# Kernel optimization log

Measured on AMD Instinct MI355X. Metric: run time of the kernel, lower is better.

## Reference

```python
import jax, jax.numpy as jnp
import numpy as np

EPS = 1e-8
LN_EPS = 1e-5  # torch LayerNorm default


def _ln(x, axes):
    m = jnp.mean(x, axis=axes, keepdims=True)
    v = jnp.var(x, axis=axes, keepdims=True)
    return (x - m) * jax.lax.rsqrt(v + LN_EPS)


def _l2(x):
    # sqrt(sum(x^2, -1, keepdim=True))
    return jnp.sqrt(jnp.sum(x * x, axis=-1, keepdims=True))


def _get_zs(x, Wk, bk, Wv, bv):
    # x: [B,L,Din]
    z = jax.nn.elu(x @ Wk.T + bk)                         # [B,L,D]
    s = jnp.einsum('blp,blq->blpq', z, x @ Wv.T + bv)     # [B,L,D,D]
    z = _ln(jnp.cumsum(z, axis=1) + EPS, -1)
    s = _ln(jnp.cumsum(s, axis=1) + EPS, (-2, -1))
    return z, s


def setup_inputs() -> dict:
    key = jax.random.key(0)
    ks = jax.random.split(key, 10)
    B, L, Din, D, U, PL, SL = 32, 200, 256, 64, 10000, 8, 8
    f32 = jnp.float32
    return {
        'user_id': jax.random.randint(ks[0], (B,), 0, U + 1),
        'seqs_emb': jax.random.normal(ks[1], (B, L, Din), dtype=f32),
        'P': jax.random.normal(ks[2], (B, PL, Din), dtype=f32),
        'S': jax.random.normal(ks[3], (B, SL, Din), dtype=f32),
        'prev_z': jax.random.normal(ks[4], (U + 1, D), dtype=f32),
        'prev_s': jax.random.normal(ks[5], (U + 1, D, D), dtype=f32),
        'Wq': jax.random.normal(ks[6], (D, Din), dtype=f32) / Din,
        'bq': jnp.zeros((D,), f32),
        'Wk': jax.random.normal(ks[7], (D, Din), dtype=f32) / Din,
        'bk': jnp.zeros((D,), f32),
        'Wv': jax.random.normal(ks[8], (D, Din), dtype=f32) / Din,
        'bv': jnp.zeros((D,), f32),
    }


def reference(user_id, seqs_emb, P, S, prev_z, prev_s, Wq, bq, Wk, bk, Wv, bv):
    sg = jax.lax.stop_gradient
    q = jax.nn.elu(seqs_emb @ Wq.T + bq)                  # [B,L,D]
    nq = q / sg(_l2(q) + EPS)
    z, s = _get_zs(seqs_emb, Wk, bk, Wv, bv)
    # plasticity prompt P: add last-step state
    Pz, Ps = _get_zs(P, Wk, bk, Wv, bv)
    z = z + Pz[:, -1:, :]
    s = s + Ps[:, -1:, :, :]
    NAM = _ln(s / sg(_l2(z)[..., None] + EPS) + EPS, (-2, -1))  # [B,L,D,D]
    NA = jnp.einsum('blp,blpq->blq', nq, NAM)
    # per-user recurrent history (use_history=True), with stability prompt S
    pz = prev_z[user_id]                                  # [B,D]
    ps = prev_s[user_id]                                  # [B,D,D]
    mask = (jnp.sum(pz, axis=-1) != 0).astype(NA.dtype)   # [B]
    Sz, Ss = _get_zs(S, Wk, bk, Wv, bv)
    zu = pz + Sz[:, -1, :]
    su = ps + Ss[:, -1, :, :]
    prev_NAM = su / sg(_l2(zu)[..., None] + EPS)          # [B,D,D]
    prev_NA = jnp.einsum('blp,bpq->blq', nq, prev_NAM) * mask[:, None, None]
    NA = _ln(NA + prev_NA, -1)                            # NA_layernorm (dropout p=0)
    std = jnp.std(q / jnp.maximum(z, 1e-6), ddof=1)       # torch.std is unbiased
    return NA, std
```

## Files before the change

kernel.cpp:

```cpp
#include <hip/hip_runtime.h>
#include <math.h>

#define B_   32
#define L_   200
#define DIN_ 256
#define D_   64
#define PL_  8

#define OFF_WT    0
#define OFF_Q     49152
#define OFF_NQ    458752
#define OFF_Z     868352
#define OFF_V     1277952
#define OFF_SZ    1687552
#define OFF_SV    1693952
#define OFF_SNQ   1700352
#define OFF_PZL   1706752
#define OFF_PSL   1708800
#define OFF_PNAM  1839872
#define OFF_MPS2  1970944
#define OFF_H     1970976
#define OFF_C     1977376
#define OFF_CM    1983776
#define OFF_CR    1990176
#define OFF_CCP   1996576
#define OFF_SYR   2002976
#define OFF_SY2R  2009376
#define OFF_ZC    2015776
#define OFF_CP    2425376
#define OFF_T1    2450976
#define OFF_T2    2860576
#define OFF_NAP   3270176

__device__ __forceinline__ float wsum(float x){
#pragma unroll
  for (int o = 32; o > 0; o >>= 1) x += __shfl_xor(x, o, 64);
  return x;
}
__device__ __forceinline__ float eluf(float x){ return x > 0.f ? x : expm1f(x); }

__global__ __launch_bounds__(256) void k_transpose(const float* __restrict__ Wq,
    const float* __restrict__ Wk, const float* __restrict__ Wv, float* __restrict__ wt){
  int idx = blockIdx.x*256 + threadIdx.x;
  if (idx >= 3*16384) return;
  int m = idx >> 14, r = idx & 16383, i = r >> 6, d = r & 63;
  const float* W = (m==0) ? Wq : ((m==1) ? Wk : Wv);
  wt[m*16384 + i*64 + d] = W[d*256 + i];
}

__global__ __launch_bounds__(256) void k_qzv(const float* __restrict__ x, const float* __restrict__ Wt,
    const float* __restrict__ bq, const float* __restrict__ bk, const float* __restrict__ bv,
    float* __restrict__ q, float* __restrict__ nq, float* __restrict__ z, float* __restrict__ v,
    float* __restrict__ sz, float* __restrict__ sv, float* __restrict__ snq){
  __shared__ float xs[16*256];
  int row0 = blockIdx.x * 16;
  int tid = threadIdx.x, d = tid & 63, g = tid >> 6;
  for (int k = tid; k < 4096; k += 256) xs[k] = x[row0*256 + k];
  __syncthreads();
  const float* Wtq = Wt;
  const float* Wtk = Wt + 16384;
  const float* Wtv = Wt + 32768;
  float aq[4] = {0,0,0,0}, ak[4] = {0,0,0,0}, av[4] = {0,0,0,0};
  for (int i = 0; i < 256; i++){
    float wq = Wtq[i*64+d], wk = Wtk[i*64+d], wv = Wtv[i*64+d];
#pragma unroll
    for (int j = 0; j < 4; j++){
      float xv = xs[(g+4*j)*256 + i];
      aq[j] = fmaf(xv, wq, aq[j]);
      ak[j] = fmaf(xv, wk, ak[j]);
      av[j] = fmaf(xv, wv, av[j]);
    }
  }
  float bqd = bq[d], bkd = bk[d], bvd = bv[d];
#pragma unroll
  for (int j = 0; j < 4; j++){
    int r = row0 + g + 4*j;
    float qv = eluf(aq[j] + bqd);
    float zv = eluf(ak[j] + bkd);
    float vv = av[j] + bvd;
    float sq2 = wsum(qv*qv);
    float sq1 = wsum(qv);
    float szv = wsum(zv);
    float svv = wsum(vv);
    float inv = 1.f / (sqrtf(sq2) + 1e-8f);
    q[r*64+d] = qv; nq[r*64+d] = qv*inv; z[r*64+d] = zv; v[r*64+d] = vv;
    if (d == 0){ sz[r] = szv; sv[r] = svv; snq[r] = sq1*inv; }
  }
}

__global__ __launch_bounds__(256) void k_prompt(const float* __restrict__ P, const float* __restrict__ Sp,
    const int* __restrict__ uid, const float* __restrict__ prev_z, const float* __restrict__ prev_s,
    const float* __restrict__ Wt, const float* __restrict__ bk, const float* __restrict__ bv,
    float* __restrict__ PzL, float* __restrict__ PsL, float* __restrict__ mps2, float* __restrict__ pNAM){
  int g = blockIdx.x, b = g & 31, path = g >> 5;
  int tid = threadIdx.x;
  __shared__ float xs[2048];
  __shared__ float zs[512], vs[512];
  __shared__ float red[4];
  __shared__ float facs;
  const float* src = path ? Sp : P;
  for (int k = tid; k < 2048; k += 256) xs[k] = src[b*2048 + k];
  __syncthreads();
  const float* Wtk = Wt + 16384;
  const float* Wtv = Wt + 32768;
  for (int idx = tid; idx < 512; idx += 256){
    int t = idx >> 6, d = idx & 63;
    float ak = 0.f, av = 0.f;
    for (int i = 0; i < 256; i++){
      float xv = xs[t*256+i];
      ak = fmaf(xv, Wtk[i*64+d], ak);
      av = fmaf(xv, Wtv[i*64+d], av);
    }
    zs[idx] = eluf(ak + bk[d]); vs[idx] = av + bv[d];
  }
  __syncthreads();
  float spv[16];
  float l1 = 0.f, l2 = 0.f;
  int p = tid >> 2, q0 = (tid & 3) * 16;
#pragma unroll
  for (int k = 0; k < 16; k++){
    int qq = q0 + k;
    float sp = 0.f;
#pragma unroll
    for (int t = 0; t < 8; t++) sp = fmaf(zs[t*64+p], vs[t*64+qq], sp);
    spv[k] = sp; l1 += sp; l2 += sp*sp;
  }
  float tot0, tot1;
  {
    float val = wsum(l1);
    if ((tid & 63) == 0) red[tid >> 6] = val;
    __syncthreads();
    tot0 = red[0] + red[1] + red[2] + red[3];
    __syncthreads();
    val = wsum(l2);
    if ((tid & 63) == 0) red[tid >> 6] = val;
    __syncthreads();
    tot1 = red[0] + red[1] + red[2] + red[3];
  }
  float mP = tot0 * (1.f/4096.f);
  float varP = tot1 * (1.f/4096.f) - mP*mP;
  float invv = rsqrtf(varP + 1e-5f);
  if (path == 0){
    if (tid == 0) mps2[b] = varP * invv * invv;
    if (tid < 64){
      int d = tid;
      float zc = 0.f;
#pragma unroll
      for (int t = 0; t < 8; t++) zc += zs[t*64+d];
      float s1 = wsum(zc), s2 = wsum(zc*zc);
      float mz = s1*(1.f/64.f), vz = s2*(1.f/64.f) - mz*mz;
      PzL[b*64+d] = (zc - mz) * rsqrtf(vz + 1e-5f);
    }
#pragma unroll
    for (int k = 0; k < 16; k++){
      int o = p*64 + q0 + k;
      PsL[b*4096 + o] = (spv[k] - mP) * invv;
    }
  } else {
    int u = uid[b];
    if (tid < 64){
      int d = tid;
      float zc = 0.f;
#pragma unroll
      for (int t = 0; t < 8; t++) zc += zs[t*64+d];
      float s1 = wsum(zc), s2 = wsum(zc*zc);
      float mz = s1*(1.f/64.f), vz = s2*(1.f/64.f) - mz*mz;
      float szl = (zc - mz) * rsqrtf(vz + 1e-5f);
      float pzv = prev_z[u*64 + d];
      float zu = pzv + szl;
      float zl2 = wsum(zu*zu);
      float psumv = wsum(pzv);
      float fac = ((psumv != 0.f) ? 1.f : 0.f) / (sqrtf(zl2) + 1e-8f);
      if (d == 0) facs = fac;
    }
    __syncthreads();
    float fac = facs;
    const float* psrow = prev_s + (size_t)u * 4096;
#pragma unroll
    for (int k = 0; k < 16; k++){
      int o = p*64 + q0 + k;
      pNAM[b*4096 + o] = (psrow[o] + (spv[k] - mP) * invv) * fac;
    }
  }
}

__global__ __launch_bounds__(256) void k_gram64(const float* __restrict__ z, const float* __restrict__ v,
    const float* __restrict__ nq,
    float* __restrict__ colpart, float* __restrict__ harr, float* __restrict__ NAP){
  __shared__ float smem[20480];
  float* zlT = smem;
  float* vlT = smem + 4096;
  float* nlT = smem + 8192;
  float* ztT = smem + 12288;
  float* vtT = smem + 16384;
  int bid = blockIdx.x;
  int b = bid / 10, pi = bid % 10;
  int rt, ct;
  if (pi < 1){ rt = 0; ct = 0; }
  else if (pi < 3){ rt = 1; ct = pi - 1; }
  else if (pi < 6){ rt = 2; ct = pi - 3; }
  else { rt = 3; ct = pi - 6; }
  int l0 = rt*64, t0 = ct*64;
  int tid = threadIdx.x;
  const float* zb = z + b*12800;
  const float* vb = v + b*12800;
  const float* nb = nq + b*12800;
  {
    int r = tid & 63, kq = tid >> 6;
    int l = l0 + r, t = t0 + r;
    bool lv = l < L_, tv = t < L_;
#pragma unroll
    for (int m = 0; m < 4; m++){
      int k0 = kq*16 + m*4;
      float4 zr4 = lv ? *(const float4*)(zb + l*64 + k0) : make_float4(0,0,0,0);
      float4 vr4 = lv ? *(const float4*)(vb + l*64 + k0) : make_float4(0,0,0,0);
      float4 nr4 = lv ? *(const float4*)(nb + l*64 + k0) : make_float4(0,0,0,0);
      float4 zc4 = tv ? *(const float4*)(zb + t*64 + k0) : make_float4(0,0,0,0);
      float4 vc4 = tv ? *(const float4*)(vb + t*64 + k0) : make_float4(0,0,0,0);
      zlT[(k0+0)*64+r]=zr4.x; zlT[(k0+1)*64+r]=zr4.y; zlT[(k0+2)*64+r]=zr4.z; zlT[(k0+3)*64+r]=zr4.w;
      vlT[(k0+0)*64+r]=vr4.x; vlT[(k0+1)*64+r]=vr4.y; vlT[(k0+2)*64+r]=vr4.z; vlT[(k0+3)*64+r]=vr4.w;
      nlT[(k0+0)*64+r]=nr4.x; nlT[(k0+1)*64+r]=nr4.y; nlT[(k0+2)*64+r]=nr4.z; nlT[(k0+3)*64+r]=nr4.w;
      ztT[(k0+0)*64+r]=zc4.x; ztT[(k0+1)*64+r]=zc4.y; ztT[(k0+2)*64+r]=zc4.z; ztT[(k0+3)*64+r]=zc4.w;
      vtT[(k0+0)*64+r]=vc4.x; vtT[(k0+1)*64+r]=vc4.y; vtT[(k0+2)*64+r]=vc4.z; vtT[(k0+3)*64+r]=vc4.w;
    }
  }
  __syncthreads();
  int rg = tid >> 4, cg = tid & 15;
  int r0 = rg*4, c0 = cg*4;
  float az[16], av[16], an[16];
#pragma unroll
  for (int i = 0; i < 16; i++){ az[i]=0.f; av[i]=0.f; an[i]=0.f; }
  for (int k = 0; k < 64; k++){
    float4 zr4 = *(const float4*)&zlT[k*64 + r0];
    float4 vr4 = *(const float4*)&vlT[k*64 + r0];
    float4 nr4 = *(const float4*)&nlT[k*64 + r0];
    float4 zc4 = *(const float4*)&ztT[k*64 + c0];
    float4 vc4 = *(const float4*)&vtT[k*64 + c0];
    float zr[4] = {zr4.x, zr4.y, zr4.z, zr4.w};
    float vr[4] = {vr4.x, vr4.y, vr4.z, vr4.w};
    float nr[4] = {nr4.x, nr4.y, nr4.z, nr4.w};
    float zc[4] = {zc4.x, zc4.y, zc4.z, zc4.w};
    float vc[4] = {vc4.x, vc4.y, vc4.z, vc4.w};
#pragma unroll
    for (int i = 0; i < 4; i++){
#pragma unroll
      for (int j = 0; j < 4; j++){
        az[i*4+j] = fmaf(zr[i], zc[j], az[i*4+j]);
        av[i*4+j] = fmaf(vr[i], vc[j], av[i*4+j]);
        an[i*4+j] = fmaf(nr[i], zc[j], an[i*4+j]);
      }
    }
  }
  bool diag = (rt == ct);
  float prow[4];
#pragma unroll
  for (int i = 0; i < 4; i++){
    float s = 0.f;
#pragma unroll
    for (int j = 0; j < 4; j++){
      bool keep = !diag || (c0 + j <= r0 + i);
      if (keep) s += az[i*4+j] * av[i*4+j];
    }
    prow[i] = s;
  }
#pragma unroll
  for (int o = 1; o < 16; o <<= 1){
#pragma unroll
    for (int i = 0; i < 4; i++) prow[i] += __shfl_xor(prow[i], o, 64);
  }
  if (cg == 0){
#pragma unroll
    for (int i = 0; i < 4; i++){
      int l = l0 + r0 + i;
      if (l < L_) colpart[(b*L_ + l)*4 + ct] = prow[i];
    }
  }
  if (diag && rg == cg){
#pragma unroll
    for (int i = 0; i < 4; i++){
      int l = l0 + r0 + i;
      if (l < L_) harr[b*L_ + l] = az[i*4+i] * av[i*4+i];
    }
  }
  __syncthreads();
  float* scsT = nlT;
#pragma unroll
  for (int j = 0; j < 4; j++){
    int c = c0 + j;
    float m0 = (!diag || c <= r0+0) ? an[0*4+j] : 0.f;
    float m1 = (!diag || c <= r0+1) ? an[1*4+j] : 0.f;
    float m2 = (!diag || c <= r0+2) ? an[2*4+j] : 0.f;
    float m3 = (!diag || c <= r0+3) ? an[3*4+j] : 0.f;
    *(float4*)&scsT[c*64 + r0] = make_float4(m0, m1, m2, m3);
  }
  __syncthreads();
  int d0 = c0;
  float o4[16];
#pragma unroll
  for (int i = 0; i < 16; i++) o4[i] = 0.f;
#pragma unroll 2
  for (int c = 0; c < 64; c++){
    float4 s4 = *(const float4*)&scsT[c*64 + r0];
    int t = t0 + c; if (t > L_-1) t = L_-1;
    float4 v4 = *(const float4*)(vb + t*64 + d0);
    float sv[4] = {s4.x, s4.y, s4.z, s4.w};
    float vv[4] = {v4.x, v4.y, v4.z, v4.w};
#pragma unroll
    for (int i = 0; i < 4; i++){
#pragma unroll
      for (int j = 0; j < 4; j++) o4[i*4+j] = fmaf(sv[i], vv[j], o4[i*4+j]);
    }
  }
  float* nap = NAP + ((size_t)((b*4 + rt)*4 + ct))*4096;
#pragma unroll
  for (int i = 0; i < 4; i++)
    *(float4*)&nap[(r0+i)*64 + d0] = make_float4(o4[i*4+0], o4[i*4+1], o4[i*4+2], o4[i*4+3]);
}

#define PADK 68
__global__ __launch_bounds__(256) void k_t12(const float* __restrict__ z, const float* __restrict__ v,
    const float* __restrict__ nq, const float* __restrict__ PsL, const float* __restrict__ pNAM,
    float* __restrict__ carr, float* __restrict__ T1, float* __restrict__ T2){
  int b = blockIdx.x / 7, rtile = blockIdx.x % 7;
  int l0 = rtile * 32;
  int tid = threadIdx.x;
  __shared__ float zl[32*PADK], vl[32*PADK];
  __shared__ float nqt[32*65];
  for (int k = tid; k < 2048; k += 256){
    int r = k >> 6, d = k & 63, lr = l0 + r;
    bool ok = lr < L_;
    zl[r*PADK+d]  = ok ? z[(b*L_+lr)*64 + d] : 0.f;
    vl[r*PADK+d]  = ok ? v[(b*L_+lr)*64 + d] : 0.f;
    nqt[r*65+d]   = ok ? nq[(b*L_+lr)*64 + d] : 0.f;
  }
  __syncthreads();
  {
    int w = tid >> 6, lane = tid & 63;
    float wacc[8] = {0,0,0,0,0,0,0,0};
    const float* psb = PsL + b*4096 + lane*64;
    for (int qq = 0; qq < 64; qq += 4){
      float4 p4 = *(const float4*)(psb + qq);
#pragma unroll
      for (int r8 = 0; r8 < 8; r8++){
        float4 v4 = *(const float4*)&vl[(w*8+r8)*PADK+qq];
        wacc[r8] += p4.x*v4.x + p4.y*v4.y + p4.z*v4.z + p4.w*v4.w;
      }
    }
#pragma unroll
    for (int r8 = 0; r8 < 8; r8++){
      int rr = w*8 + r8, l = l0 + rr;
      float c = wsum(zl[rr*PADK+lane] * wacc[r8]);
      if (lane == 0 && l < L_) carr[b*L_ + l] = c;
    }
  }
  int r = tid & 31, c8 = tid >> 5, c0 = c8 * 8;
  float t1a[8] = {0,0,0,0,0,0,0,0}, t2a[8] = {0,0,0,0,0,0,0,0};
  const float* psm = PsL + b*4096;
  const float* pnm = pNAM + b*4096;
  for (int pp = 0; pp < 64; pp++){
    float nv = nqt[r*65 + pp];
    float4 a0 = *(const float4*)(psm + pp*64 + c0);
    float4 a1 = *(const float4*)(psm + pp*64 + c0 + 4);
    float4 b0 = *(const float4*)(pnm + pp*64 + c0);
    float4 b1 = *(const float4*)(pnm + pp*64 + c0 + 4);
    t1a[0] = fmaf(nv, a0.x, t1a[0]); t1a[1] = fmaf(nv, a0.y, t1a[1]);
    t1a[2] = fmaf(nv, a0.z, t1a[2]); t1a[3] = fmaf(nv, a0.w, t1a[3]);
    t1a[4] = fmaf(nv, a1.x, t1a[4]); t1a[5] = fmaf(nv, a1.y, t1a[5]);
    t1a[6] = fmaf(nv, a1.z, t1a[6]); t1a[7] = fmaf(nv, a1.w, t1a[7]);
    t2a[0] = fmaf(nv, b0.x, t2a[0]); t2a[1] = fmaf(nv, b0.y, t2a[1]);
    t2a[2] = fmaf(nv, b0.z, t2a[2]); t2a[3] = fmaf(nv, b0.w, t2a[3]);
    t2a[4] = fmaf(nv, b1.x, t2a[4]); t2a[5] = fmaf(nv, b1.y, t2a[5]);
    t2a[6] = fmaf(nv, b1.z, t2a[6]); t2a[7] = fmaf(nv, b1.w, t2a[7]);
  }
  int l = l0 + r;
  if (l < L_){
    float* t1p = T1 + (b*L_+l)*64 + c0;
    float* t2p = T2 + (b*L_+l)*64 + c0;
    *(float4*)(t1p)     = make_float4(t1a[0], t1a[1], t1a[2], t1a[3]);
    *(float4*)(t1p + 4) = make_float4(t1a[4], t1a[5], t1a[6], t1a[7]);
    *(float4*)(t2p)     = make_float4(t2a[0], t2a[1], t2a[2], t2a[3]);
    *(float4*)(t2p + 4) = make_float4(t2a[4], t2a[5], t2a[6], t2a[7]);
  }
}

__global__ __launch_bounds__(64) void k_cumsum(const float* __restrict__ z,
    const float* __restrict__ sz, const float* __restrict__ sv,
    const float* __restrict__ colpart, const float* __restrict__ harr, const float* __restrict__ carr,
    float* __restrict__ Zcum, float* __restrict__ cM, float* __restrict__ cR, float* __restrict__ cC){
  int b = blockIdx.x, lane = threadIdx.x;
  const float* zb = z + b*12800;
  float* Zb = Zcum + b*12800;
  float Zc = 0.f;
  for (int l = 0; l < 200; l += 4){
    float a0 = zb[(l+0)*64+lane];
    float a1 = zb[(l+1)*64+lane];
    float a2 = zb[(l+2)*64+lane];
    float a3 = zb[(l+3)*64+lane];
    Zc += a0; Zb[(l+0)*64+lane] = Zc;
    Zc += a1; Zb[(l+1)*64+lane] = Zc;
    Zc += a2; Zb[(l+2)*64+lane] = Zc;
    Zc += a3; Zb[(l+3)*64+lane] = Zc;
  }
  float carryM = 0.f, carryR = 0.f, carryC = 0.f;
#pragma unroll
  for (int c = 0; c < 4; c++){
    int l = c*64 + lane;
    bool valid = l < 200;
    int row = b*200 + l;
    float tcol = 0.f;
    if (valid){
      int ltile = l >> 6;
#pragma unroll
      for (int j = 0; j < 4; j++)
        if (j <= ltile) tcol += colpart[row*4 + j];
    }
    float tm = valid ? sz[row]*sv[row] : 0.f;
    float tr = valid ? 2.f*tcol - harr[row] : 0.f;
    float tc = valid ? carr[row] : 0.f;
#pragma unroll
    for (int o = 1; o < 64; o <<= 1){
      float y0 = __shfl_up(tm, o, 64);
      float y1 = __shfl_up(tr, o, 64);
      float y2 = __shfl_up(tc, o, 64);
      if (lane >= o){ tm += y0; tr += y1; tc += y2; }
    }
    tm += carryM; tr += carryR; tc += carryC;
    if (valid){ cM[row] = tm; cR[row] = tr; cC[row] = tc; }
    carryM = __shfl(tm, 63, 64);
    carryR = __shfl(tr, 63, 64);
    carryC = __shfl(tc, 63, 64);
  }
}

__global__ __launch_bounds__(64) void k_finred(const float* __restrict__ q, const float* __restrict__ Zcum,
    const float* __restrict__ PzL, const float* __restrict__ mps2, const float* __restrict__ snq,
    const float* __restrict__ cM, const float* __restrict__ cR, const float* __restrict__ cC,
    const float* __restrict__ T1, const float* __restrict__ T2, const float* __restrict__ NAP,
    float* __restrict__ out, float* __restrict__ Syr, float* __restrict__ Sy2r){
  int row = blockIdx.x;
  int b = row / 200, l = row % 200;
  int lane = threadIdx.x;
  int rt = l >> 6, r = l & 63;
  const float* np_ = NAP + ((size_t)((b*4 + rt)*4))*4096 + r*64 + lane;
  float acc = 0.f;
  for (int ct = 0; ct <= rt; ct++) acc += np_[ct*4096];
  float zc = Zcum[row*64 + lane];
  float s1 = wsum(zc), s2 = wsum(zc*zc);
  float mz = s1*(1.f/64.f), vz = s2*(1.f/64.f) - mz*mz;
  float zf = (zc - mz) * rsqrtf(vz + 1e-5f) + PzL[b*64 + lane];
  float zl2 = wsum(zf*zf);
  float a = sqrtf(zl2) + 1e-8f;
  float m = cM[row] * (1.f/4096.f);
  float var = cR[row] * (1.f/4096.f) - m*m;
  float inv = rsqrtf(var + 1e-5f);
  float varT = inv*inv*var + 2.f*inv*cC[row]*(1.f/4096.f) + mps2[b];
  float invT = rsqrtf(varT + 1e-5f*a*a);
  float cAv = invT*inv;
  float cBv = invT*inv*m*snq[row];
  float cCv = invT;
  float y = q[row*64 + lane] / fmaxf(zf, 1e-6f);
  float ys = wsum(y), ys2 = wsum(y*y);
  if (lane == 0){ Syr[row] = ys; Sy2r[row] = ys2; }
  float NA1 = cAv*acc - cBv + cCv*T1[row*64 + lane] + T2[row*64 + lane];
  float r1 = wsum(NA1), r2 = wsum(NA1*NA1);
  float mm = r1*(1.f/64.f), vv = r2*(1.f/64.f) - mm*mm;
  out[row*64 + lane] = (NA1 - mm) * rsqrtf(vv + 1e-5f);
}

__global__ __launch_bounds__(256) void k_std(const float* __restrict__ Syr, const float* __restrict__ Sy2r,
    float* __restrict__ out){
  __shared__ float redA[4], redB[4];
  int tid = threadIdx.x, lane = tid & 63, g = tid >> 6;
  float a = 0.f, b2 = 0.f;
  for (int i = tid; i < 6400; i += 256){ a += Syr[i]; b2 += Sy2r[i]; }
  a = wsum(a); b2 = wsum(b2);
  if (lane == 0){ redA[g] = a; redB[g] = b2; }
  __syncthreads();
  if (tid == 0){
    float A = redA[0]+redA[1]+redA[2]+redA[3];
    float B2 = redB[0]+redB[1]+redB[2]+redB[3];
    const float N = 409600.f;
    float var = (B2 - A*A/N) / (N - 1.f);
    out[409600] = sqrtf(fmaxf(var, 0.f));
  }
}

extern "C" void kernel_launch(void* const* d_in, const int* in_sizes, int n_in,
                              void* d_out, int out_size, void* d_ws, size_t ws_size,
                              hipStream_t stream) {
  const int*   uid    = (const int*)d_in[0];
  const float* seqs   = (const float*)d_in[1];
  const float* P      = (const float*)d_in[2];
  const float* S      = (const float*)d_in[3];
  const float* prev_z = (const float*)d_in[4];
  const float* prev_s = (const float*)d_in[5];
  const float* Wq     = (const float*)d_in[6];
  const float* bq     = (const float*)d_in[7];
  const float* Wk     = (const float*)d_in[8];
  const float* bk     = (const float*)d_in[9];
  const float* Wv     = (const float*)d_in[10];
  const float* bv     = (const float*)d_in[11];
  float* w   = (float*)d_ws;
  float* out = (float*)d_out;

  k_transpose<<<192, 256, 0, stream>>>(Wq, Wk, Wv, w + OFF_WT);
  k_qzv<<<400, 256, 0, stream>>>(seqs, w + OFF_WT, bq, bk, bv,
      w + OFF_Q, w + OFF_NQ, w + OFF_Z, w + OFF_V, w + OFF_SZ, w + OFF_SV, w + OFF_SNQ);
  k_prompt<<<64, 256, 0, stream>>>(P, S, uid, prev_z, prev_s, w + OFF_WT, bk, bv,
      w + OFF_PZL, w + OFF_PSL, w + OFF_MPS2, w + OFF_PNAM);
  k_gram64<<<B_*10, 256, 0, stream>>>(w + OFF_Z, w + OFF_V, w + OFF_NQ,
      w + OFF_CP, w + OFF_H, w + OFF_NAP);
  k_t12<<<B_*7, 256, 0, stream>>>(w + OFF_Z, w + OFF_V, w + OFF_NQ,
      w + OFF_PSL, w + OFF_PNAM,
      w + OFF_C, w + OFF_T1, w + OFF_T2);
  k_cumsum<<<32, 64, 0, stream>>>(w + OFF_Z, w + OFF_SZ, w + OFF_SV,
      w + OFF_CP, w + OFF_H, w + OFF_C,
      w + OFF_ZC, w + OFF_CM, w + OFF_CR, w + OFF_CCP);
  k_finred<<<6400, 64, 0, stream>>>(w + OFF_Q, w + OFF_ZC,
      w + OFF_PZL, w + OFF_MPS2, w + OFF_SNQ,
      w + OFF_CM, w + OFF_CR, w + OFF_CCP,
      w + OFF_T1, w + OFF_T2, w + OFF_NAP,
      out, w + OFF_SYR, w + OFF_SY2R);
  k_std<<<1, 256, 0, stream>>>(w + OFF_SYR, w + OFF_SY2R, out);
}
```

Baseline: 139.3 us.

## Fuse eight kernels into two stages with atomic-ticket last-block finalization

```diff
diff --git a/kernel.cpp b/kernel.cpp
--- a/kernel.cpp
+++ b/kernel.cpp
@@ -3,34 +3,27 @@
 
 #define B_   32
 #define L_   200
-#define DIN_ 256
-#define D_   64
-#define PL_  8
-
-#define OFF_WT    0
-#define OFF_Q     49152
-#define OFF_NQ    458752
-#define OFF_Z     868352
-#define OFF_V     1277952
-#define OFF_SZ    1687552
-#define OFF_SV    1693952
-#define OFF_SNQ   1700352
-#define OFF_PZL   1706752
-#define OFF_PSL   1708800
-#define OFF_PNAM  1839872
-#define OFF_MPS2  1970944
-#define OFF_H     1970976
-#define OFF_C     1977376
-#define OFF_CM    1983776
-#define OFF_CR    1990176
-#define OFF_CCP   1996576
-#define OFF_SYR   2002976
-#define OFF_SY2R  2009376
-#define OFF_ZC    2015776
-#define OFF_CP    2425376
-#define OFF_T1    2450976
-#define OFF_T2    2860576
-#define OFF_NAP   3270176
+
+#define OFF_Q     0
+#define OFF_NQ    409600
+#define OFF_Z     819200
+#define OFF_V     1228800
+#define OFF_SZ    1638400
+#define OFF_SV    1644800
+#define OFF_SNQ   1651200
+#define OFF_PZL   1657600
+#define OFF_PSL   1659648
+#define OFF_PNAM  1790720
+#define OFF_MPS2  1921792
+#define OFF_H     1921824
+#define OFF_C     1928224
+#define OFF_CP    1934624
+#define OFF_T1    1960224
+#define OFF_T2    2369824
+#define OFF_NAP   2779424
+#define OFF_SYB   4876576
+#define OFF_SY2B  4876608
+#define OFF_CNT   4876640
 
 __device__ __forceinline__ float wsum(float x){
 #pragma unroll
@@ -39,80 +32,114 @@
 }
 __device__ __forceinline__ float eluf(float x){ return x > 0.f ? x : expm1f(x); }
 
-__global__ __launch_bounds__(256) void k_transpose(const float* __restrict__ Wq,
-    const float* __restrict__ Wk, const float* __restrict__ Wv, float* __restrict__ wt){
-  int idx = blockIdx.x*256 + threadIdx.x;
-  if (idx >= 3*16384) return;
-  int m = idx >> 14, r = idx & 16383, i = r >> 6, d = r & 63;
-  const float* W = (m==0) ? Wq : ((m==1) ? Wk : Wv);
-  wt[m*16384 + i*64 + d] = W[d*256 + i];
-}
-
-__global__ __launch_bounds__(256) void k_qzv(const float* __restrict__ x, const float* __restrict__ Wt,
+__global__ __launch_bounds__(256) void k_stage1(
+    const float* __restrict__ x, const float* __restrict__ P, const float* __restrict__ Sp,
+    const int* __restrict__ uid, const float* __restrict__ prev_z, const float* __restrict__ prev_s,
+    const float* __restrict__ Wq, const float* __restrict__ Wk, const float* __restrict__ Wv,
     const float* __restrict__ bq, const float* __restrict__ bk, const float* __restrict__ bv,
     float* __restrict__ q, float* __restrict__ nq, float* __restrict__ z, float* __restrict__ v,
-    float* __restrict__ sz, float* __restrict__ sv, float* __restrict__ snq){
-  __shared__ float xs[16*256];
-  int row0 = blockIdx.x * 16;
-  int tid = threadIdx.x, d = tid & 63, g = tid >> 6;
-  for (int k = tid; k < 4096; k += 256) xs[k] = x[row0*256 + k];
-  __syncthreads();
-  const float* Wtq = Wt;
-  const float* Wtk = Wt + 16384;
-  const float* Wtv = Wt + 32768;
-  float aq[4] = {0,0,0,0}, ak[4] = {0,0,0,0}, av[4] = {0,0,0,0};
-  for (int i = 0; i < 256; i++){
-    float wq = Wtq[i*64+d], wk = Wtk[i*64+d], wv = Wtv[i*64+d];
-#pragma unroll
-    for (int j = 0; j < 4; j++){
-      float xv = xs[(g+4*j)*256 + i];
-      aq[j] = fmaf(xv, wq, aq[j]);
-      ak[j] = fmaf(xv, wk, ak[j]);
-      av[j] = fmaf(xv, wv, av[j]);
-    }
-  }
-  float bqd = bq[d], bkd = bk[d], bvd = bv[d];
-#pragma unroll
-  for (int j = 0; j < 4; j++){
-    int r = row0 + g + 4*j;
-    float qv = eluf(aq[j] + bqd);
-    float zv = eluf(ak[j] + bkd);
-    float vv = av[j] + bvd;
-    float sq2 = wsum(qv*qv);
-    float sq1 = wsum(qv);
-    float szv = wsum(zv);
-    float svv = wsum(vv);
+    float* __restrict__ sz, float* __restrict__ sv, float* __restrict__ snq,
+    float* __restrict__ PzL, float* __restrict__ PsL, float* __restrict__ mps2,
+    float* __restrict__ pNAM, int* __restrict__ counters){
+  __shared__ float smem[14720];
+  int tid = threadIdx.x, bid = blockIdx.x;
+  if (bid == 0 && tid < 64) counters[tid] = 0;
+  if (bid < 200){
+    float* xs = smem;
+    float* wl = smem + 8192;
+    int row0 = bid * 32;
+    for (int k = tid; k < 8192; k += 256) xs[k] = x[row0*256 + k];
+    int r = tid >> 3, dg = tid & 7, d0 = dg * 8;
+    float aq[8] = {0,0,0,0,0,0,0,0};
+    float ak[8] = {0,0,0,0,0,0,0,0};
+    float av[8] = {0,0,0,0,0,0,0,0};
+    for (int c = 0; c < 8; c++){
+      __syncthreads();
+      for (int s = tid; s < 6144; s += 256){
+        int il = s & 31, d_ = (s >> 5) & 63, m = s >> 11;
+        const float* W = (m == 0) ? Wq : ((m == 1) ? Wk : Wv);
+        wl[m*2176 + il*68 + d_] = W[d_*256 + c*32 + il];
+      }
+      __syncthreads();
+      const float* xr = xs + r*256 + c*32;
+      for (int il = 0; il < 32; il++){
+        float xv = xr[il];
+        const float* wr = wl + il*68 + d0;
+        float4 a0 = *(const float4*)(wr);
+        float4 a1 = *(const float4*)(wr + 4);
+        float4 b0 = *(const float4*)(wr + 2176);
+        float4 b1 = *(const float4*)(wr + 2180);
+        float4 c0 = *(const float4*)(wr + 4352);
+        float4 c1 = *(const float4*)(wr + 4356);
+        aq[0]=fmaf(xv,a0.x,aq[0]); aq[1]=fmaf(xv,a0.y,aq[1]); aq[2]=fmaf(xv,a0.z,aq[2]); aq[3]=fmaf(xv,a0.w,aq[3]);
+        aq[4]=fmaf(xv,a1.x,aq[4]); aq[5]=fmaf(xv,a1.y,aq[5]); aq[6]=fmaf(xv,a1.z,aq[6]); aq[7]=fmaf(xv,a1.w,aq[7]);
+        ak[0]=fmaf(xv,b0.x,ak[0]); ak[1]=fmaf(xv,b0.y,ak[1]); ak[2]=fmaf(xv,b0.z,ak[2]); ak[3]=fmaf(xv,b0.w,ak[3]);
+        ak[4]=fmaf(xv,b1.x,ak[4]); ak[5]=fmaf(xv,b1.y,ak[5]); ak[6]=fmaf(xv,b1.z,ak[6]); ak[7]=fmaf(xv,b1.w,ak[7]);
+        av[0]=fmaf(xv,c0.x,av[0]); av[1]=fmaf(xv,c0.y,av[1]); av[2]=fmaf(xv,c0.z,av[2]); av[3]=fmaf(xv,c0.w,av[3]);
+        av[4]=fmaf(xv,c1.x,av[4]); av[5]=fmaf(xv,c1.y,av[5]); av[6]=fmaf(xv,c1.z,av[6]); av[7]=fmaf(xv,c1.w,av[7]);
+      }
+    }
+    float qv[8], zv[8], vv[8];
+    float sq2 = 0.f, sq1 = 0.f, szp = 0.f, svp = 0.f;
+#pragma unroll
+    for (int j = 0; j < 8; j++){
+      qv[j] = eluf(aq[j] + bq[d0+j]);
+      zv[j] = eluf(ak[j] + bk[d0+j]);
+      vv[j] = av[j] + bv[d0+j];
+      sq2 += qv[j]*qv[j]; sq1 += qv[j]; szp += zv[j]; svp += vv[j];
+    }
+#pragma unroll
+    for (int o = 1; o < 8; o <<= 1){
+      sq2 += __shfl_xor(sq2, o, 64);
+      sq1 += __shfl_xor(sq1, o, 64);
+      szp += __shfl_xor(szp, o, 64);
+      svp += __shfl_xor(svp, o, 64);
+    }
     float inv = 1.f / (sqrtf(sq2) + 1e-8f);
-    q[r*64+d] = qv; nq[r*64+d] = qv*inv; z[r*64+d] = zv; v[r*64+d] = vv;
-    if (d == 0){ sz[r] = szv; sv[r] = svv; snq[r] = sq1*inv; }
-  }
-}
-
-__global__ __launch_bounds__(256) void k_prompt(const float* __restrict__ P, const float* __restrict__ Sp,
-    const int* __restrict__ uid, const float* __restrict__ prev_z, const float* __restrict__ prev_s,
-    const float* __restrict__ Wt, const float* __restrict__ bk, const float* __restrict__ bv,
-    float* __restrict__ PzL, float* __restrict__ PsL, float* __restrict__ mps2, float* __restrict__ pNAM){
-  int g = blockIdx.x, b = g & 31, path = g >> 5;
-  int tid = threadIdx.x;
-  __shared__ float xs[2048];
-  __shared__ float zs[512], vs[512];
-  __shared__ float red[4];
-  __shared__ float facs;
+    int row = row0 + r;
+    *(float4*)(q + row*64 + d0)     = make_float4(qv[0],qv[1],qv[2],qv[3]);
+    *(float4*)(q + row*64 + d0 + 4) = make_float4(qv[4],qv[5],qv[6],qv[7]);
+    *(float4*)(nq + row*64 + d0)     = make_float4(qv[0]*inv,qv[1]*inv,qv[2]*inv,qv[3]*inv);
+    *(float4*)(nq + row*64 + d0 + 4) = make_float4(qv[4]*inv,qv[5]*inv,qv[6]*inv,qv[7]*inv);
+    *(float4*)(z + row*64 + d0)     = make_float4(zv[0],zv[1],zv[2],zv[3]);
+    *(float4*)(z + row*64 + d0 + 4) = make_float4(zv[4],zv[5],zv[6],zv[7]);
+    *(float4*)(v + row*64 + d0)     = make_float4(vv[0],vv[1],vv[2],vv[3]);
+    *(float4*)(v + row*64 + d0 + 4) = make_float4(vv[4],vv[5],vv[6],vv[7]);
+    if (dg == 0){ sz[row] = szp; sv[row] = svp; snq[row] = sq1*inv; }
+    return;
+  }
+  int g = bid - 200, b = g & 31, path = g >> 5;
+  float* xs = smem;
+  float* wl = smem + 2048;
+  float* zs = smem + 6400;
+  float* vs = smem + 6912;
+  float* red = smem + 7424;
+  float* facs = smem + 7428;
   const float* src = path ? Sp : P;
   for (int k = tid; k < 2048; k += 256) xs[k] = src[b*2048 + k];
-  __syncthreads();
-  const float* Wtk = Wt + 16384;
-  const float* Wtv = Wt + 32768;
-  for (int idx = tid; idx < 512; idx += 256){
-    int t = idx >> 6, d = idx & 63;
-    float ak = 0.f, av = 0.f;
-    for (int i = 0; i < 256; i++){
-      float xv = xs[t*256+i];
-      ak = fmaf(xv, Wtk[i*64+d], ak);
-      av = fmaf(xv, Wtv[i*64+d], av);
-    }
-    zs[idx] = eluf(ak + bk[d]); vs[idx] = av + bv[d];
-  }
+  int t0i = tid >> 6, d0i = tid & 63;
+  float accK0 = 0.f, accV0 = 0.f, accK1 = 0.f, accV1 = 0.f;
+  for (int c = 0; c < 8; c++){
+    __syncthreads();
+    for (int s = tid; s < 4096; s += 256){
+      int il = s & 31, d_ = (s >> 5) & 63, m = s >> 11;
+      const float* W = m ? Wv : Wk;
+      wl[m*2176 + il*68 + d_] = W[d_*256 + c*32 + il];
+    }
+    __syncthreads();
+    const float* x0 = xs + t0i*256 + c*32;
+    const float* x1 = xs + (t0i+4)*256 + c*32;
+    for (int il = 0; il < 32; il++){
+      float wk_ = wl[il*68 + d0i];
+      float wv_ = wl[2176 + il*68 + d0i];
+      accK0 = fmaf(x0[il], wk_, accK0);
+      accV0 = fmaf(x0[il], wv_, accV0);
+      accK1 = fmaf(x1[il], wk_, accK1);
+      accV1 = fmaf(x1[il], wv_, accV1);
+    }
+  }
+  zs[tid]     = eluf(accK0 + bk[d0i]); vs[tid]     = accV0 + bv[d0i];
+  zs[tid+256] = eluf(accK1 + bk[d0i]); vs[tid+256] = accV1 + bv[d0i];
   __syncthreads();
   float spv[16];
   float l1 = 0.f, l2 = 0.f;
@@ -171,10 +198,10 @@
       float zl2 = wsum(zu*zu);
       float psumv = wsum(pzv);
       float fac = ((psumv != 0.f) ? 1.f : 0.f) / (sqrtf(zl2) + 1e-8f);
-      if (d == 0) facs = fac;
-    }
-    __syncthreads();
-    float fac = facs;
+      if (d == 0) facs[0] = fac;
+    }
+    __syncthreads();
+    float fac = facs[0];
     const float* psrow = prev_s + (size_t)u * 4096;
 #pragma unroll
     for (int k = 0; k < 16; k++){
@@ -184,304 +211,306 @@
   }
 }
 
-__global__ __launch_bounds__(256) void k_gram64(const float* __restrict__ z, const float* __restrict__ v,
-    const float* __restrict__ nq,
-    float* __restrict__ colpart, float* __restrict__ harr, float* __restrict__ NAP){
+#define PADK 68
+__global__ __launch_bounds__(256) void k_stage2(
+    const float* __restrict__ z, const float* __restrict__ v, const float* __restrict__ nq,
+    const float* __restrict__ q, const float* __restrict__ sz, const float* __restrict__ sv,
+    const float* __restrict__ snq, const float* __restrict__ PsL, const float* __restrict__ pNAM,
+    const float* __restrict__ PzL, const float* __restrict__ mps2,
+    float* __restrict__ colpart, float* __restrict__ harr, float* __restrict__ carr,
+    float* __restrict__ T1, float* __restrict__ T2, float* __restrict__ NAP,
+    float* __restrict__ Syb, float* __restrict__ Sy2b,
+    int* __restrict__ counters, float* __restrict__ out){
   __shared__ float smem[20480];
-  float* zlT = smem;
-  float* vlT = smem + 4096;
-  float* nlT = smem + 8192;
-  float* ztT = smem + 12288;
-  float* vtT = smem + 16384;
-  int bid = blockIdx.x;
-  int b = bid / 10, pi = bid % 10;
-  int rt, ct;
-  if (pi < 1){ rt = 0; ct = 0; }
-  else if (pi < 3){ rt = 1; ct = pi - 1; }
-  else if (pi < 6){ rt = 2; ct = pi - 3; }
-  else { rt = 3; ct = pi - 6; }
-  int l0 = rt*64, t0 = ct*64;
-  int tid = threadIdx.x;
+  __shared__ int ticket_s;
+  int tid = threadIdx.x, bid = blockIdx.x;
+  int b = bid / 17, pi = bid % 17;
   const float* zb = z + b*12800;
   const float* vb = v + b*12800;
   const float* nb = nq + b*12800;
+  if (pi < 10){
+    float* zlT = smem;
+    float* vlT = smem + 4096;
+    float* nlT = smem + 8192;
+    float* ztT = smem + 12288;
+    float* vtT = smem + 16384;
+    int rt, ct;
+    if (pi < 1){ rt = 0; ct = 0; }
+    else if (pi < 3){ rt = 1; ct = pi - 1; }
+    else if (pi < 6){ rt = 2; ct = pi - 3; }
+    else { rt = 3; ct = pi - 6; }
+    int l0 = rt*64, t0 = ct*64;
+    {
+      int r = tid & 63, kq = tid >> 6;
+      int l = l0 + r, t = t0 + r;
+      bool lv = l < L_, tv = t < L_;
+#pragma unroll
+      for (int m = 0; m < 4; m++){
+        int k0 = kq*16 + m*4;
+        float4 zr4 = lv ? *(const float4*)(zb + l*64 + k0) : make_float4(0,0,0,0);
+        float4 vr4 = lv ? *(const float4*)(vb + l*64 + k0) : make_float4(0,0,0,0);
+        float4 nr4 = lv ? *(const float4*)(nb + l*64 + k0) : make_float4(0,0,0,0);
+        float4 zc4 = tv ? *(const float4*)(zb + t*64 + k0) : make_float4(0,0,0,0);
+        float4 vc4 = tv ? *(const float4*)(vb + t*64 + k0) : make_float4(0,0,0,0);
+        zlT[(k0+0)*64+r]=zr4.x; zlT[(k0+1)*64+r]=zr4.y; zlT[(k0+2)*64+r]=zr4.z; zlT[(k0+3)*64+r]=zr4.w;
+        vlT[(k0+0)*64+r]=vr4.x; vlT[(k0+1)*64+r]=vr4.y; vlT[(k0+2)*64+r]=vr4.z; vlT[(k0+3)*64+r]=vr4.w;
+        nlT[(k0+0)*64+r]=nr4.x; nlT[(k0+1)*64+r]=nr4.y; nlT[(k0+2)*64+r]=nr4.z; nlT[(k0+3)*64+r]=nr4.w;
+        ztT[(k0+0)*64+r]=zc4.x; ztT[(k0+1)*64+r]=zc4.y; ztT[(k0+2)*64+r]=zc4.z; ztT[(k0+3)*64+r]=zc4.w;
+        vtT[(k0+0)*64+r]=vc4.x; vtT[(k0+1)*64+r]=vc4.y; vtT[(k0+2)*64+r]=vc4.z; vtT[(k0+3)*64+r]=vc4.w;
+      }
+    }
+    __syncthreads();
+    int rg = tid >> 4, cg = tid & 15;
+    int r0 = rg*4, c0 = cg*4;
+    float az[16], av[16], an[16];
+#pragma unroll
+    for (int i = 0; i < 16; i++){ az[i]=0.f; av[i]=0.f; an[i]=0.f; }
+    for (int k = 0; k < 64; k++){
+      float4 zr4 = *(const float4*)&zlT[k*64 + r0];
+      float4 vr4 = *(const float4*)&vlT[k*64 + r0];
+      float4 nr4 = *(const float4*)&nlT[k*64 + r0];
+      float4 zc4 = *(const float4*)&ztT[k*64 + c0];
+      float4 vc4 = *(const float4*)&vtT[k*64 + c0];
+      float zr[4] = {zr4.x, zr4.y, zr4.z, zr4.w};
+      float vr[4] = {vr4.x, vr4.y, vr4.z, vr4.w};
+      float nr[4] = {nr4.x, nr4.y, nr4.z, nr4.w};
+      float zc[4] = {zc4.x, zc4.y, zc4.z, zc4.w};
+      float vc[4] = {vc4.x, vc4.y, vc4.z, vc4.w};
+#pragma unroll
+      for (int i = 0; i < 4; i++){
+#pragma unroll
+        for (int j = 0; j < 4; j++){
+          az[i*4+j] = fmaf(zr[i], zc[j], az[i*4+j]);
+          av[i*4+j] = fmaf(vr[i], vc[j], av[i*4+j]);
+          an[i*4+j] = fmaf(nr[i], zc[j], an[i*4+j]);
+        }
+      }
+    }
+    bool diag = (rt == ct);
+    float prow[4];
+#pragma unroll
+    for (int i = 0; i < 4; i++){
+      float s = 0.f;
+#pragma unroll
+      for (int j = 0; j < 4; j++){
+        bool keep = !diag || (c0 + j <= r0 + i);
+        if (keep) s += az[i*4+j] * av[i*4+j];
+      }
+      prow[i] = s;
+    }
+#pragma unroll
+    for (int o = 1; o < 16; o <<= 1){
+#pragma unroll
+      for (int i = 0; i < 4; i++) prow[i] += __shfl_xor(prow[i], o, 64);
+    }
+    if (cg == 0){
+#pragma unroll
+      for (int i = 0; i < 4; i++){
+        int l = l0 + r0 + i;
+        if (l < L_) colpart[(b*L_ + l)*4 + ct] = prow[i];
+      }
+    }
+    if (diag && rg == cg){
+#pragma unroll
+      for (int i = 0; i < 4; i++){
+        int l = l0 + r0 + i;
+        if (l < L_) harr[b*L_ + l] = az[i*4+i] * av[i*4+i];
+      }
+    }
+    __syncthreads();
+    float* scsT = nlT;
+#pragma unroll
+    for (int j = 0; j < 4; j++){
+      int c = c0 + j;
+      float m0 = (!diag || c <= r0+0) ? an[0*4+j] : 0.f;
+      float m1 = (!diag || c <= r0+1) ? an[1*4+j] : 0.f;
+      float m2 = (!diag || c <= r0+2) ? an[2*4+j] : 0.f;
+      float m3 = (!diag || c <= r0+3) ? an[3*4+j] : 0.f;
+      *(float4*)&scsT[c*64 + r0] = make_float4(m0, m1, m2, m3);
+    }
+    __syncthreads();
+    {
+      int d0 = c0;
+      float o4[16];
+#pragma unroll
+      for (int i = 0; i < 16; i++) o4[i] = 0.f;
+#pragma unroll 2
+      for (int c = 0; c < 64; c++){
+        float4 s4 = *(const float4*)&scsT[c*64 + r0];
+        int t = t0 + c; if (t > L_-1) t = L_-1;
+        float4 v4 = *(const float4*)(vb + t*64 + d0);
+        float sv4[4] = {s4.x, s4.y, s4.z, s4.w};
+        float vv4[4] = {v4.x, v4.y, v4.z, v4.w};
+#pragma unroll
+        for (int i = 0; i < 4; i++){
+#pragma unroll
+          for (int j = 0; j < 4; j++) o4[i*4+j] = fmaf(sv4[i], vv4[j], o4[i*4+j]);
+        }
+      }
+      float* nap = NAP + ((size_t)((b*4 + rt)*4 + ct))*4096;
+#pragma unroll
+      for (int i = 0; i < 4; i++)
+        *(float4*)&nap[(r0+i)*64 + d0] = make_float4(o4[i*4+0], o4[i*4+1], o4[i*4+2], o4[i*4+3]);
+    }
+  } else {
+    float* zl  = smem;
+    float* vl  = smem + 2176;
+    float* nqt = smem + 4352;
+    int rtile = pi - 10;
+    int l0 = rtile * 32;
+    for (int k = tid; k < 2048; k += 256){
+      int r = k >> 6, d = k & 63, lr = l0 + r;
+      bool ok = lr < L_;
+      zl[r*PADK+d] = ok ? zb[lr*64 + d] : 0.f;
+      vl[r*PADK+d] = ok ? vb[lr*64 + d] : 0.f;
+      nqt[r*65+d]  = ok ? nb[lr*64 + d] : 0.f;
+    }
+    __syncthreads();
+    {
+      int w = tid >> 6, lane = tid & 63;
+      float wacc[8] = {0,0,0,0,0,0,0,0};
+      const float* psb = PsL + b*4096 + lane*64;
+      for (int qq = 0; qq < 64; qq += 4){
+        float4 p4 = *(const float4*)(psb + qq);
+#pragma unroll
+        for (int r8 = 0; r8 < 8; r8++){
+          float4 v4 = *(const float4*)&vl[(w*8+r8)*PADK+qq];
+          wacc[r8] += p4.x*v4.x + p4.y*v4.y + p4.z*v4.z + p4.w*v4.w;
+        }
+      }
+#pragma unroll
+      for (int r8 = 0; r8 < 8; r8++){
+        int rr = w*8 + r8, l = l0 + rr;
+        float c = wsum(zl[rr*PADK+lane] * wacc[r8]);
+        if (lane == 0 && l < L_) carr[b*L_ + l] = c;
+      }
+    }
+    {
+      int r = tid & 31, c8 = tid >> 5, c0 = c8 * 8;
+      float t1a[8] = {0,0,0,0,0,0,0,0}, t2a[8] = {0,0,0,0,0,0,0,0};
+      const float* psm = PsL + b*4096;
+      const float* pnm = pNAM + b*4096;
+      for (int pp = 0; pp < 64; pp++){
+        float nv = nqt[r*65 + pp];
+        float4 a0 = *(const float4*)(psm + pp*64 + c0);
+        float4 a1 = *(const float4*)(psm + pp*64 + c0 + 4);
+        float4 b0 = *(const float4*)(pnm + pp*64 + c0);
+        float4 b1 = *(const float4*)(pnm + pp*64 + c0 + 4);
+        t1a[0]=fmaf(nv,a0.x,t1a[0]); t1a[1]=fmaf(nv,a0.y,t1a[1]); t1a[2]=fmaf(nv,a0.z,t1a[2]); t1a[3]=fmaf(nv,a0.w,t1a[3]);
+        t1a[4]=fmaf(nv,a1.x,t1a[4]); t1a[5]=fmaf(nv,a1.y,t1a[5]); t1a[6]=fmaf(nv,a1.z,t1a[6]); t1a[7]=fmaf(nv,a1.w,t1a[7]);
+        t2a[0]=fmaf(nv,b0.x,t2a[0]); t2a[1]=fmaf(nv,b0.y,t2a[1]); t2a[2]=fmaf(nv,b0.z,t2a[2]); t2a[3]=fmaf(nv,b0.w,t2a[3]);
+        t2a[4]=fmaf(nv,b1.x,t2a[4]); t2a[5]=fmaf(nv,b1.y,t2a[5]); t2a[6]=fmaf(nv,b1.z,t2a[6]); t2a[7]=fmaf(nv,b1.w,t2a[7]);
+      }
+      int l = l0 + r;
+      if (l < L_){
+        float* t1p = T1 + (b*L_+l)*64 + c0;
+        float* t2p = T2 + (b*L_+l)*64 + c0;
+        *(float4*)(t1p)     = make_float4(t1a[0], t1a[1], t1a[2], t1a[3]);
+        *(float4*)(t1p + 4) = make_float4(t1a[4], t1a[5], t1a[6], t1a[7]);
+        *(float4*)(t2p)     = make_float4(t2a[0], t2a[1], t2a[2], t2a[3]);
+        *(float4*)(t2p + 4) = make_float4(t2a[4], t2a[5], t2a[6], t2a[7]);
+      }
+    }
+  }
+  __syncthreads();
+  if (tid == 0)
+    ticket_s = __hip_atomic_fetch_add(&counters[b], 1, __ATOMIC_ACQ_REL, __HIP_MEMORY_SCOPE_AGENT);
+  __syncthreads();
+  if (ticket_s != 16) return;
+  float* zc  = smem;
+  float* scm = smem + 12800;
+  float* scr = smem + 13000;
+  float* scc = smem + 13200;
+  float* sred  = smem + 13400;
+  float* s2red = smem + 13404;
+  int w = tid >> 6, d = tid & 63;
   {
-    int r = tid & 63, kq = tid >> 6;
-    int l = l0 + r, t = t0 + r;
-    bool lv = l < L_, tv = t < L_;
-#pragma unroll
-    for (int m = 0; m < 4; m++){
-      int k0 = kq*16 + m*4;
-      float4 zr4 = lv ? *(const float4*)(zb + l*64 + k0) : make_float4(0,0,0,0);
-      float4 vr4 = lv ? *(const float4*)(vb + l*64 + k0) : make_float4(0,0,0,0);
-      float4 nr4 = lv ? *(const float4*)(nb + l*64 + k0) : make_float4(0,0,0,0);
-      float4 zc4 = tv ? *(const float4*)(zb + t*64 + k0) : make_float4(0,0,0,0);
-      float4 vc4 = tv ? *(const float4*)(vb + t*64 + k0) : make_float4(0,0,0,0);
-      zlT[(k0+0)*64+r]=zr4.x; zlT[(k0+1)*64+r]=zr4.y; zlT[(k0+2)*64+r]=zr4.z; zlT[(k0+3)*64+r]=zr4.w;
-      vlT[(k0+0)*64+r]=vr4.x; vlT[(k0+1)*64+r]=vr4.y; vlT[(k0+2)*64+r]=vr4.z; vlT[(k0+3)*64+r]=vr4.w;
-      nlT[(k0+0)*64+r]=nr4.x; nlT[(k0+1)*64+r]=nr4.y; nlT[(k0+2)*64+r]=nr4.z; nlT[(k0+3)*64+r]=nr4.w;
-      ztT[(k0+0)*64+r]=zc4.x; ztT[(k0+1)*64+r]=zc4.y; ztT[(k0+2)*64+r]=zc4.z; ztT[(k0+3)*64+r]=zc4.w;
-      vtT[(k0+0)*64+r]=vc4.x; vtT[(k0+1)*64+r]=vc4.y; vtT[(k0+2)*64+r]=vc4.z; vtT[(k0+3)*64+r]=vc4.w;
+    float run = 0.f;
+    for (int i = 0; i < 50; i++){
+      int l = w*50 + i;
+      run += zb[l*64 + d];
+      zc[l*64 + d] = run;
     }
   }
   __syncthreads();
-  int rg = tid >> 4, cg = tid & 15;
-  int r0 = rg*4, c0 = cg*4;
-  float az[16], av[16], an[16];
-#pragma unroll
-  for (int i = 0; i < 16; i++){ az[i]=0.f; av[i]=0.f; an[i]=0.f; }
-  for (int k = 0; k < 64; k++){
-    float4 zr4 = *(const float4*)&zlT[k*64 + r0];
-    float4 vr4 = *(const float4*)&vlT[k*64 + r0];
-    float4 nr4 = *(const float4*)&nlT[k*64 + r0];
-    float4 zc4 = *(const float4*)&ztT[k*64 + c0];
-    float4 vc4 = *(const float4*)&vtT[k*64 + c0];
-    float zr[4] = {zr4.x, zr4.y, zr4.z, zr4.w};
-    float vr[4] = {vr4.x, vr4.y, vr4.z, vr4.w};
-    float nr[4] = {nr4.x, nr4.y, nr4.z, nr4.w};
-    float zc[4] = {zc4.x, zc4.y, zc4.z, zc4.w};
-    float vc[4] = {vc4.x, vc4.y, vc4.z, vc4.w};
-#pragma unroll
-    for (int i = 0; i < 4; i++){
-#pragma unroll
-      for (int j = 0; j < 4; j++){
-        az[i*4+j] = fmaf(zr[i], zc[j], az[i*4+j]);
-        av[i*4+j] = fmaf(vr[i], vc[j], av[i*4+j]);
-        an[i*4+j] = fmaf(nr[i], zc[j], an[i*4+j]);
-      }
-    }
-  }
-  bool diag = (rt == ct);
-  float prow[4];
-#pragma unroll
-  for (int i = 0; i < 4; i++){
-    float s = 0.f;
-#pragma unroll
-    for (int j = 0; j < 4; j++){
-      bool keep = !diag || (c0 + j <= r0 + i);
-      if (keep) s += az[i*4+j] * av[i*4+j];
-    }
-    prow[i] = s;
-  }
-#pragma unroll
-  for (int o = 1; o < 16; o <<= 1){
-#pragma unroll
-    for (int i = 0; i < 4; i++) prow[i] += __shfl_xor(prow[i], o, 64);
-  }
-  if (cg == 0){
-#pragma unroll
-    for (int i = 0; i < 4; i++){
-      int l = l0 + r0 + i;
-      if (l < L_) colpart[(b*L_ + l)*4 + ct] = prow[i];
-    }
-  }
-  if (diag && rg == cg){
-#pragma unroll
-    for (int i = 0; i < 4; i++){
-      int l = l0 + r0 + i;
-      if (l < L_) harr[b*L_ + l] = az[i*4+i] * av[i*4+i];
+  float off = 0.f;
+  for (int w2 = 0; w2 < w; w2++) off += zc[(w2*50 + 49)*64 + d];
+  if (w == 0){
+    int lane = d;
+    float carryM = 0.f, carryR = 0.f, carryC = 0.f;
+    for (int c2 = 0; c2 < 4; c2++){
+      int l = c2*64 + lane;
+      bool valid = l < 200;
+      int row = b*200 + l;
+      float tcol = 0.f;
+      if (valid){
+        int lt = l >> 6;
+#pragma unroll
+        for (int j = 0; j < 4; j++) if (j <= lt) tcol += colpart[row*4 + j];
+      }
+      float tm = valid ? sz[row]*sv[row] : 0.f;
+      float tr = valid ? 2.f*tcol - harr[row] : 0.f;
+      float tc = valid ? carr[row] : 0.f;
+#pragma unroll
+      for (int o = 1; o < 64; o <<= 1){
+        float y0 = __shfl_up(tm, o, 64);
+        float y1 = __shfl_up(tr, o, 64);
+        float y2 = __shfl_up(tc, o, 64);
+        if (lane >= o){ tm += y0; tr += y1; tc += y2; }
+      }
+      tm += carryM; tr += carryR; tc += carryC;
+      if (valid){ scm[l] = tm; scr[l] = tr; scc[l] = tc; }
+      carryM = __shfl(tm, 63, 64);
+      carryR = __shfl(tr, 63, 64);
+      carryC = __shfl(tc, 63, 64);
     }
   }
   __syncthreads();
-  float* scsT = nlT;
-#pragma unroll
-  for (int j = 0; j < 4; j++){
-    int c = c0 + j;
-    float m0 = (!diag || c <= r0+0) ? an[0*4+j] : 0.f;
-    float m1 = (!diag || c <= r0+1) ? an[1*4+j] : 0.f;
-    float m2 = (!diag || c <= r0+2) ? an[2*4+j] : 0.f;
-    float m3 = (!diag || c <= r0+3) ? an[3*4+j] : 0.f;
-    *(float4*)&scsT[c*64 + r0] = make_float4(m0, m1, m2, m3);
-  }
-  __syncthreads();
-  int d0 = c0;
-  float o4[16];
-#pragma unroll
-  for (int i = 0; i < 16; i++) o4[i] = 0.f;
-#pragma unroll 2
-  for (int c = 0; c < 64; c++){
-    float4 s4 = *(const float4*)&scsT[c*64 + r0];
-    int t = t0 + c; if (t > L_-1) t = L_-1;
-    float4 v4 = *(const float4*)(vb + t*64 + d0);
-    float sv[4] = {s4.x, s4.y, s4.z, s4.w};
-    float vv[4] = {v4.x, v4.y, v4.z, v4.w};
-#pragma unroll
-    for (int i = 0; i < 4; i++){
-#pragma unroll
-      for (int j = 0; j < 4; j++) o4[i*4+j] = fmaf(sv[i], vv[j], o4[i*4+j]);
-    }
-  }
-  float* nap = NAP + ((size_t)((b*4 + rt)*4 + ct))*4096;
-#pragma unroll
-  for (int i = 0; i < 4; i++)
-    *(float4*)&nap[(r0+i)*64 + d0] = make_float4(o4[i*4+0], o4[i*4+1], o4[i*4+2], o4[i*4+3]);
-}
-
-#define PADK 68
-__global__ __launch_bounds__(256) void k_t12(const float* __restrict__ z, const float* __restrict__ v,
-    const float* __restrict__ nq, const float* __restrict__ PsL, const float* __restrict__ pNAM,
-    float* __restrict__ carr, float* __restrict__ T1, float* __restrict__ T2){
-  int b = blockIdx.x / 7, rtile = blockIdx.x % 7;
-  int l0 = rtile * 32;
-  int tid = threadIdx.x;
-  __shared__ float zl[32*PADK], vl[32*PADK];
-  __shared__ float nqt[32*65];
-  for (int k = tid; k < 2048; k += 256){
-    int r = k >> 6, d = k & 63, lr = l0 + r;
-    bool ok = lr < L_;
-    zl[r*PADK+d]  = ok ? z[(b*L_+lr)*64 + d] : 0.f;
-    vl[r*PADK+d]  = ok ? v[(b*L_+lr)*64 + d] : 0.f;
-    nqt[r*65+d]   = ok ? nq[(b*L_+lr)*64 + d] : 0.f;
-  }
-  __syncthreads();
-  {
-    int w = tid >> 6, lane = tid & 63;
-    float wacc[8] = {0,0,0,0,0,0,0,0};
-    const float* psb = PsL + b*4096 + lane*64;
-    for (int qq = 0; qq < 64; qq += 4){
-      float4 p4 = *(const float4*)(psb + qq);
-#pragma unroll
-      for (int r8 = 0; r8 < 8; r8++){
-        float4 v4 = *(const float4*)&vl[(w*8+r8)*PADK+qq];
-        wacc[r8] += p4.x*v4.x + p4.y*v4.y + p4.z*v4.z + p4.w*v4.w;
-      }
-    }
-#pragma unroll
-    for (int r8 = 0; r8 < 8; r8++){
-      int rr = w*8 + r8, l = l0 + rr;
-      float c = wsum(zl[rr*PADK+lane] * wacc[r8]);
-      if (lane == 0 && l < L_) carr[b*L_ + l] = c;
-    }
-  }
-  int r = tid & 31, c8 = tid >> 5, c0 = c8 * 8;
-  float t1a[8] = {0,0,0,0,0,0,0,0}, t2a[8] = {0,0,0,0,0,0,0,0};
-  const float* psm = PsL + b*4096;
-  const float* pnm = pNAM + b*4096;
-  for (int pp = 0; pp < 64; pp++){
-    float nv = nqt[r*65 + pp];
-    float4 a0 = *(const float4*)(psm + pp*64 + c0);
-    float4 a1 = *(const float4*)(psm + pp*64 + c0 + 4);
-    float4 b0 = *(const float4*)(pnm + pp*64 + c0);
-    float4 b1 = *(const float4*)(pnm + pp*64 + c0 + 4);
-    t1a[0] = fmaf(nv, a0.x, t1a[0]); t1a[1] = fmaf(nv, a0.y, t1a[1]);
-    t1a[2] = fmaf(nv, a0.z, t1a[2]); t1a[3] = fmaf(nv, a0.w, t1a[3]);
-    t1a[4] = fmaf(nv, a1.x, t1a[4]); t1a[5] = fmaf(nv, a1.y, t1a[5]);
-    t1a[6] = fmaf(nv, a1.z, t1a[6]); t1a[7] = fmaf(nv, a1.w, t1a[7]);
-    t2a[0] = fmaf(nv, b0.x, t2a[0]); t2a[1] = fmaf(nv, b0.y, t2a[1]);
-    t2a[2] = fmaf(nv, b0.z, t2a[2]); t2a[3] = fmaf(nv, b0.w, t2a[3]);
-    t2a[4] = fmaf(nv, b1.x, t2a[4]); t2a[5] = fmaf(nv, b1.y, t2a[5]);
-    t2a[6] = fmaf(nv, b1.z, t2a[6]); t2a[7] = fmaf(nv, b1.w, t2a[7]);
-  }
-  int l = l0 + r;
-  if (l < L_){
-    float* t1p = T1 + (b*L_+l)*64 + c0;
-    float* t2p = T2 + (b*L_+l)*64 + c0;
-    *(float4*)(t1p)     = make_float4(t1a[0], t1a[1], t1a[2], t1a[3]);
-    *(float4*)(t1p + 4) = make_float4(t1a[4], t1a[5], t1a[6], t1a[7]);
-    *(float4*)(t2p)     = make_float4(t2a[0], t2a[1], t2a[2], t2a[3]);
-    *(float4*)(t2p + 4) = make_float4(t2a[4], t2a[5], t2a[6], t2a[7]);
-  }
-}
-
-__global__ __launch_bounds__(64) void k_cumsum(const float* __restrict__ z,
-    const float* __restrict__ sz, const float* __restrict__ sv,
-    const float* __restrict__ colpart, const float* __restrict__ harr, const float* __restrict__ carr,
-    float* __restrict__ Zcum, float* __restrict__ cM, float* __restrict__ cR, float* __restrict__ cC){
-  int b = blockIdx.x, lane = threadIdx.x;
-  const float* zb = z + b*12800;
-  float* Zb = Zcum + b*12800;
-  float Zc = 0.f;
-  for (int l = 0; l < 200; l += 4){
-    float a0 = zb[(l+0)*64+lane];
-    float a1 = zb[(l+1)*64+lane];
-    float a2 = zb[(l+2)*64+lane];
-    float a3 = zb[(l+3)*64+lane];
-    Zc += a0; Zb[(l+0)*64+lane] = Zc;
-    Zc += a1; Zb[(l+1)*64+lane] = Zc;
-    Zc += a2; Zb[(l+2)*64+lane] = Zc;
-    Zc += a3; Zb[(l+3)*64+lane] = Zc;
-  }
-  float carryM = 0.f, carryR = 0.f, carryC = 0.f;
-#pragma unroll
-  for (int c = 0; c < 4; c++){
-    int l = c*64 + lane;
-    bool valid = l < 200;
-    int row = b*200 + l;
-    float tcol = 0.f;
-    if (valid){
-      int ltile = l >> 6;
-#pragma unroll
-      for (int j = 0; j < 4; j++)
-        if (j <= ltile) tcol += colpart[row*4 + j];
-    }
-    float tm = valid ? sz[row]*sv[row] : 0.f;
-    float tr = valid ? 2.f*tcol - harr[row] : 0.f;
-    float tc = valid ? carr[row] : 0.f;
-#pragma unroll
-    for (int o = 1; o < 64; o <<= 1){
-      float y0 = __shfl_up(tm, o, 64);
-      float y1 = __shfl_up(tr, o, 64);
-      float y2 = __shfl_up(tc, o, 64);
-      if (lane >= o){ tm += y0; tr += y1; tc += y2; }
-    }
-    tm += carryM; tr += carryR; tc += carryC;
-    if (valid){ cM[row] = tm; cR[row] = tr; cC[row] = tc; }
-    carryM = __shfl(tm, 63, 64);
-    carryR = __shfl(tr, 63, 64);
-    carryC = __shfl(tc, 63, 64);
-  }
-}
-
-__global__ __launch_bounds__(64) void k_finred(const float* __restrict__ q, const float* __restrict__ Zcum,
-    const float* __restrict__ PzL, const float* __restrict__ mps2, const float* __restrict__ snq,
-    const float* __restrict__ cM, const float* __restrict__ cR, const float* __restrict__ cC,
-    const float* __restrict__ T1, const float* __restrict__ T2, const float* __restrict__ NAP,
-    float* __restrict__ out, float* __restrict__ Syr, float* __restrict__ Sy2r){
-  int row = blockIdx.x;
-  int b = row / 200, l = row % 200;
-  int lane = threadIdx.x;
-  int rt = l >> 6, r = l & 63;
-  const float* np_ = NAP + ((size_t)((b*4 + rt)*4))*4096 + r*64 + lane;
-  float acc = 0.f;
-  for (int ct = 0; ct <= rt; ct++) acc += np_[ct*4096];
-  float zc = Zcum[row*64 + lane];
-  float s1 = wsum(zc), s2 = wsum(zc*zc);
-  float mz = s1*(1.f/64.f), vz = s2*(1.f/64.f) - mz*mz;
-  float zf = (zc - mz) * rsqrtf(vz + 1e-5f) + PzL[b*64 + lane];
-  float zl2 = wsum(zf*zf);
-  float a = sqrtf(zl2) + 1e-8f;
-  float m = cM[row] * (1.f/4096.f);
-  float var = cR[row] * (1.f/4096.f) - m*m;
-  float inv = rsqrtf(var + 1e-5f);
-  float varT = inv*inv*var + 2.f*inv*cC[row]*(1.f/4096.f) + mps2[b];
-  float invT = rsqrtf(varT + 1e-5f*a*a);
-  float cAv = invT*inv;
-  float cBv = invT*inv*m*snq[row];
-  float cCv = invT;
-  float y = q[row*64 + lane] / fmaxf(zf, 1e-6f);
-  float ys = wsum(y), ys2 = wsum(y*y);
-  if (lane == 0){ Syr[row] = ys; Sy2r[row] = ys2; }
-  float NA1 = cAv*acc - cBv + cCv*T1[row*64 + lane] + T2[row*64 + lane];
-  float r1 = wsum(NA1), r2 = wsum(NA1*NA1);
-  float mm = r1*(1.f/64.f), vv = r2*(1.f/64.f) - mm*mm;
-  out[row*64 + lane] = (NA1 - mm) * rsqrtf(vv + 1e-5f);
-}
-
-__global__ __launch_bounds__(256) void k_std(const float* __restrict__ Syr, const float* __restrict__ Sy2r,
-    float* __restrict__ out){
-  __shared__ float redA[4], redB[4];
-  int tid = threadIdx.x, lane = tid & 63, g = tid >> 6;
-  float a = 0.f, b2 = 0.f;
-  for (int i = tid; i < 6400; i += 256){ a += Syr[i]; b2 += Sy2r[i]; }
-  a = wsum(a); b2 = wsum(b2);
-  if (lane == 0){ redA[g] = a; redB[g] = b2; }
+  float pzl = PzL[b*64 + d], mp2 = mps2[b];
+  float ys = 0.f, ys2 = 0.f;
+  for (int i = 0; i < 50; i++){
+    int l = w*50 + i, row = b*200 + l;
+    float Zc = zc[l*64 + d] + off;
+    float s1 = wsum(Zc), s2 = wsum(Zc*Zc);
+    float mz = s1*(1.f/64.f), vz = s2*(1.f/64.f) - mz*mz;
+    float zf = (Zc - mz) * rsqrtf(vz + 1e-5f) + pzl;
+    float zl2 = wsum(zf*zf);
+    float a = sqrtf(zl2) + 1e-8f;
+    float m = scm[l] * (1.f/4096.f);
+    float var = scr[l] * (1.f/4096.f) - m*m;
+    float inv = rsqrtf(var + 1e-5f);
+    float varT = inv*inv*var + 2.f*inv*scc[l]*(1.f/4096.f) + mp2;
+    float invT = rsqrtf(varT + 1e-5f*a*a);
+    float cAv = invT*inv;
+    float cBv = invT*inv*m*snq[row];
+    float cCv = invT;
+    int rt = l >> 6, rr = l & 63;
+    const float* np_ = NAP + ((size_t)(b*4 + rt))*4*4096 + rr*64 + d;
+    float acc = 0.f;
+    for (int ct = 0; ct <= rt; ct++) acc += np_[ct*4096];
+    float NA1 = cAv*acc - cBv + cCv*T1[row*64 + d] + T2[row*64 + d];
+    float r1 = wsum(NA1), r2 = wsum(NA1*NA1);
+    float mm = r1*(1.f/64.f), vv2 = r2*(1.f/64.f) - mm*mm;
+    out[row*64 + d] = (NA1 - mm) * rsqrtf(vv2 + 1e-5f);
+    float y = q[row*64 + d] / fmaxf(zf, 1e-6f);
+    ys += y;
+    ys2 = fmaf(y, y, ys2);
+  }
+  ys = wsum(ys); ys2 = wsum(ys2);
+  if (d == 0){ sred[w] = ys; s2red[w] = ys2; }
   __syncthreads();
   if (tid == 0){
-    float A = redA[0]+redA[1]+redA[2]+redA[3];
-    float B2 = redB[0]+redB[1]+redB[2]+redB[3];
-    const float N = 409600.f;
-    float var = (B2 - A*A/N) / (N - 1.f);
-    out[409600] = sqrtf(fmaxf(var, 0.f));
+    float SY = sred[0]+sred[1]+sred[2]+sred[3];
+    float SY2 = s2red[0]+s2red[1]+s2red[2]+s2red[3];
+    Syb[b] = SY; Sy2b[b] = SY2;
+    int t2 = __hip_atomic_fetch_add(&counters[32], 1, __ATOMIC_ACQ_REL, __HIP_MEMORY_SCOPE_AGENT);
+    if (t2 == 31){
+      float A = 0.f, B2 = 0.f;
+      for (int i = 0; i < 32; i++){ A += Syb[i]; B2 += Sy2b[i]; }
+      const float N = 409600.f;
+      float var = (B2 - A*A/N) / (N - 1.f);
+      out[409600] = sqrtf(fmaxf(var, 0.f));
+    }
   }
 }
 
@@ -503,23 +532,17 @@
   float* w   = (float*)d_ws;
   float* out = (float*)d_out;
 
-  k_transpose<<<192, 256, 0, stream>>>(Wq, Wk, Wv, w + OFF_WT);
-  k_qzv<<<400, 256, 0, stream>>>(seqs, w + OFF_WT, bq, bk, bv,
-      w + OFF_Q, w + OFF_NQ, w + OFF_Z, w + OFF_V, w + OFF_SZ, w + OFF_SV, w + OFF_SNQ);
-  k_prompt<<<64, 256, 0, stream>>>(P, S, uid, prev_z, prev_s, w + OFF_WT, bk, bv,
-      w + OFF_PZL, w + OFF_PSL, w + OFF_MPS2, w + OFF_PNAM);
-  k_gram64<<<B_*10, 256, 0, stream>>>(w + OFF_Z, w + OFF_V, w + OFF_NQ,
-      w + OFF_CP, w + OFF_H, w + OFF_NAP);
-  k_t12<<<B_*7, 256, 0, stream>>>(w + OFF_Z, w + OFF_V, w + OFF_NQ,
-      w + OFF_PSL, w + OFF_PNAM,
-      w + OFF_C, w + OFF_T1, w + OFF_T2);
-  k_cumsum<<<32, 64, 0, stream>>>(w + OFF_Z, w + OFF_SZ, w + OFF_SV,
+  k_stage1<<<264, 256, 0, stream>>>(seqs, P, S, uid, prev_z, prev_s,
+      Wq, Wk, Wv, bq, bk, bv,
+      w + OFF_Q, w + OFF_NQ, w + OFF_Z, w + OFF_V,
+      w + OFF_SZ, w + OFF_SV, w + OFF_SNQ,
+      w + OFF_PZL, w + OFF_PSL, w + OFF_MPS2, w + OFF_PNAM,
+      (int*)(w + OFF_CNT));
+  k_stage2<<<B_*17, 256, 0, stream>>>(w + OFF_Z, w + OFF_V, w + OFF_NQ,
+      w + OFF_Q, w + OFF_SZ, w + OFF_SV, w + OFF_SNQ,
+      w + OFF_PSL, w + OFF_PNAM, w + OFF_PZL, w + OFF_MPS2,
       w + OFF_CP, w + OFF_H, w + OFF_C,
-      w + OFF_ZC, w + OFF_CM, w + OFF_CR, w + OFF_CCP);
-  k_finred<<<6400, 64, 0, stream>>>(w + OFF_Q, w + OFF_ZC,
-      w + OFF_PZL, w + OFF_MPS2, w + OFF_SNQ,
-      w + OFF_CM, w + OFF_CR, w + OFF_CCP,
       w + OFF_T1, w + OFF_T2, w + OFF_NAP,
-      out, w + OFF_SYR, w + OFF_SY2R);
-  k_std<<<1, 256, 0, stream>>>(w + OFF_SYR, w + OFF_SY2R, out);
+      w + OFF_SYB, w + OFF_SY2B,
+      (int*)(w + OFF_CNT), out);
 }
```

New measurement: 234.4 us. 68.2% more time.
